# Kernel optimization log

Hardware: AMD Instinct MI355X
Metric: run time of the kernel (lower is better)

Reference implementation:

```python
import jax, jax.numpy as jnp
import numpy as np

IN_C = 256
INTER_C = 128


def _conv1x1(x_flat, w, b):
    # x_flat: [n, c_in, N]; w: [c_out, c_in]; b: [c_out] -> [n, c_out, N]
    return jnp.einsum('oc,bcn->bon', w, x_flat) + b[None, :, None]


def setup_inputs() -> dict:
    key = jax.random.key(0)
    ks = jax.random.split(key, 9)
    x = jax.random.normal(ks[0], (4, IN_C, 64, 64), dtype=jnp.float32)
    s_in = 1.0 / np.sqrt(IN_C)
    s_mid = 1.0 / np.sqrt(INTER_C)
    return {
        'x': x,
        'g_w': jax.random.uniform(ks[1], (INTER_C, IN_C), jnp.float32, -s_in, s_in),
        'g_b': jax.random.uniform(ks[2], (INTER_C,), jnp.float32, -s_in, s_in),
        'theta_w': jax.random.uniform(ks[3], (INTER_C, IN_C), jnp.float32, -s_in, s_in),
        'theta_b': jax.random.uniform(ks[4], (INTER_C,), jnp.float32, -s_in, s_in),
        'phi_w': jax.random.uniform(ks[5], (INTER_C, IN_C), jnp.float32, -s_in, s_in),
        'phi_b': jax.random.uniform(ks[6], (INTER_C,), jnp.float32, -s_in, s_in),
        'out_w': jax.random.uniform(ks[7], (IN_C, INTER_C), jnp.float32, -s_mid, s_mid),
        'out_b': jax.random.uniform(ks[8], (IN_C,), jnp.float32, -s_mid, s_mid),
    }


def reference(x, g_w, g_b, theta_w, theta_b, phi_w, phi_b, out_w, out_b):
    n, c, h, w = x.shape
    N = h * w
    x_flat = x.reshape(n, c, N)
    # 1x1-conv projections
    g_x = _conv1x1(x_flat, g_w, g_b).transpose(0, 2, 1)       # [n, N, ci]
    theta_x = _conv1x1(x_flat, theta_w, theta_b).transpose(0, 2, 1)  # [n, N, ci]
    phi_x = _conv1x1(x_flat, phi_w, phi_b)                    # [n, ci, N]
    # dot_product variant: pairwise weight normalized by N (no softmax)
    pairwise_weight = jnp.matmul(theta_x, phi_x) / N          # [n, N, N]
    y = jnp.matmul(pairwise_weight, g_x)                      # [n, N, ci]
    y = y.transpose(0, 2, 1)                                  # [n, ci, N]
    out = x_flat + _conv1x1(y, out_w, out_b)                  # residual
    return out.reshape(n, c, h, w)
```

## Files before the change

kernel.cpp:

```cpp
#include <hip/hip_runtime.h>
#include <hip/hip_bf16.h>


#define CC   256
#define NSP  4096
#define NB   4
#define KSPLIT 16

typedef __attribute__((ext_vector_type(8))) short bf16x8;
typedef __attribute__((ext_vector_type(4))) float f32x4;

#define F_BST  0
#define F_PART 512
#define F_WEND 1049088
#define H_XT   0
#define H_PG   4194304
#define H_TT   8388608
#define H_WST  10485760
#define H_OWH  10584064
#define H_W2   10616832

__device__ __forceinline__ unsigned short f2bf(float f) {
  __hip_bfloat16 h = __float2bfloat16(f);
  return __builtin_bit_cast(unsigned short, h);
}
__device__ __forceinline__ uint4 pack8(const unsigned short* h) {
  uint4 u;
  u.x = (unsigned)h[0] | ((unsigned)h[1] << 16);
  u.y = (unsigned)h[2] | ((unsigned)h[3] << 16);
  u.z = (unsigned)h[4] | ((unsigned)h[5] << 16);
  u.w = (unsigned)h[6] | ((unsigned)h[7] << 16);
  return u;
}

__device__ __forceinline__ void wave_gemm_bt(const unsigned short* __restrict__ A, int pitchA,
                                             const unsigned short* __restrict__ B, int pitchB,
                                             int K, int lane, f32x4 acc[4][4]) {
  int lm = lane & 15, lq = lane >> 4;
  const unsigned short* ap[4];
  const unsigned short* bp[4];
#pragma unroll
  for (int i = 0; i < 4; ++i) {
    ap[i] = A + (size_t)(i * 16 + lm) * pitchA + lq * 8;
    bp[i] = B + (size_t)(i * 16 + lm) * pitchB + lq * 8;
  }
  bf16x8 a0[4], b0[4];
#pragma unroll
  for (int i = 0; i < 4; ++i) {
    a0[i] = *(const bf16x8*)(ap[i]);
    b0[i] = *(const bf16x8*)(bp[i]);
  }
  for (int k = 32; k < K; k += 32) {
    bf16x8 a1[4], b1[4];
#pragma unroll
    for (int i = 0; i < 4; ++i) {
      a1[i] = *(const bf16x8*)(ap[i] + k);
      b1[i] = *(const bf16x8*)(bp[i] + k);
    }
#pragma unroll
    for (int mi = 0; mi < 4; ++mi)
#pragma unroll
      for (int ni = 0; ni < 4; ++ni)
        acc[mi][ni] = __builtin_amdgcn_mfma_f32_16x16x32_bf16(a0[mi], b0[ni], acc[mi][ni], 0, 0, 0);
#pragma unroll
    for (int i = 0; i < 4; ++i) { a0[i] = a1[i]; b0[i] = b1[i]; }
  }
#pragma unroll
  for (int mi = 0; mi < 4; ++mi)
#pragma unroll
    for (int ni = 0; ni < 4; ++ni)
      acc[mi][ni] = __builtin_amdgcn_mfma_f32_16x16x32_bf16(a0[mi], b0[ni], acc[mi][ni], 0, 0, 0);
}

__global__ __launch_bounds__(256) void kA(
    const float* __restrict__ g_w, const float* __restrict__ theta_w,
    const float* __restrict__ phi_w, const float* __restrict__ out_w,
    const float* __restrict__ g_b, const float* __restrict__ theta_b,
    const float* __restrict__ phi_b, const float* __restrict__ x,
    float* __restrict__ wsf, unsigned short* __restrict__ wsh) {
  __shared__ float T[64][65];
  int bid = blockIdx.x, t = threadIdx.x;
  if (bid < 1024) {
    int nt = bid & 63, ct = (bid >> 6) & 3, b = bid >> 8;
    int c0 = ct * 64, n0 = nt * 64;
    int r = t >> 2, j = t & 3;
    const float* xr = x + ((size_t)b * CC + c0 + r) * NSP + n0 + j * 16;
    float4 f0 = *(const float4*)(xr);
    float4 f1 = *(const float4*)(xr + 4);
    float4 f2 = *(const float4*)(xr + 8);
    float4 f3 = *(const float4*)(xr + 12);
    *(float4*)&T[r][j * 16 + 0]  = f0;
    *(float4*)&T[r][j * 16 + 4]  = f1;
    *(float4*)&T[r][j * 16 + 8]  = f2;
    *(float4*)&T[r][j * 16 + 12] = f3;
    __syncthreads();
    int nr = t >> 2, j2 = t & 3;
    unsigned short o[16];
#pragma unroll
    for (int i = 0; i < 16; ++i) o[i] = f2bf(T[j2 * 16 + i][nr]);
    size_t to = ((size_t)b * NSP + n0 + nr) * CC + c0 + j2 * 16;
    *(uint4*)(wsh + H_XT + to)     = pack8(o);
    *(uint4*)(wsh + H_XT + to + 8) = pack8(o + 8);
  } else if (bid < 1028) {
    int r0 = (bid - 1024) * 96;
    for (int i = 0; i < 96; ++i) {
      int rr = r0 + i;
      const float* src = (rr < 128) ? (g_w + (size_t)rr * CC)
                       : (rr < 256) ? (theta_w + (size_t)(rr - 128) * CC)
                                    : (phi_w + (size_t)(rr - 256) * CC);
      wsh[H_WST + (size_t)rr * CC + t] = f2bf(src[t]);
    }
  } else {
    for (int i = t; i < 32768; i += 256) wsh[H_OWH + i] = f2bf(out_w[i]);
    if (t < 128) {
      wsf[F_BST + t]       = g_b[t];
      wsf[F_BST + 128 + t] = theta_b[t];
      wsf[F_BST + 256 + t] = phi_b[t];
    }
  }
}

__global__ __launch_bounds__(256) void kB(const float* __restrict__ wsf,
                                          unsigned short* __restrict__ wsh) {
  __shared__ float bL[128];
  int bid = blockIdx.x;
  int b = bid / 96, rem = bid % 96;
  int r = rem >> 5, c = rem & 31;
  int t = threadIdx.x, w = t >> 6, lane = t & 63;
  int wm = w >> 1, wn = w & 1;
  int lm = lane & 15, lq = lane >> 4;
  if (t < 128) bL[t] = wsf[F_BST + r * 128 + t];
  __syncthreads();

  const unsigned short* A = wsh + H_WST + (size_t)(r * 128 + wm * 64) * CC;
  const unsigned short* B = wsh + H_XT + ((size_t)b * NSP + c * 128 + wn * 64) * CC;
  f32x4 acc[4][4] = {};
  wave_gemm_bt(A, CC, B, CC, 256, lane, acc);

  int colb = c * 128 + wn * 64;
  if (r == 1) {
    size_t tb = (size_t)b * 524288;
#pragma unroll
    for (int mi = 0; mi < 4; ++mi) {
      int p0 = wm * 64 + mi * 16 + lq * 4;
#pragma unroll
      for (int ni = 0; ni < 4; ++ni) {
        int col = colb + ni * 16 + lm;
        unsigned short u0 = f2bf(acc[mi][ni][0] + bL[p0 + 0]);
        unsigned short u1 = f2bf(acc[mi][ni][1] + bL[p0 + 1]);
        unsigned short u2 = f2bf(acc[mi][ni][2] + bL[p0 + 2]);
        unsigned short u3 = f2bf(acc[mi][ni][3] + bL[p0 + 3]);
        uint2 o;
        o.x = (unsigned)u0 | ((unsigned)u1 << 16);
        o.y = (unsigned)u2 | ((unsigned)u3 << 16);
        *(uint2*)(wsh + H_TT + tb + (size_t)col * 128 + p0) = o;
      }
    }
  } else {
    int rbase = (r == 0) ? 0 : 128;
    size_t pbo = (size_t)b * 1048576;
#pragma unroll
    for (int mi = 0; mi < 4; ++mi)
#pragma unroll
      for (int rr = 0; rr < 4; ++rr) {
        int rl = wm * 64 + mi * 16 + lq * 4 + rr;
        float bv = bL[rl];
        size_t rowo = pbo + (size_t)(rbase + rl) * NSP;
#pragma unroll
        for (int ni = 0; ni < 4; ++ni)
          wsh[H_PG + rowo + colb + ni * 16 + lm] = f2bf(acc[mi][ni][rr] + bv);
      }
  }
}

__global__ __launch_bounds__(256) void kC1(const unsigned short* __restrict__ wsh,
                                           float* __restrict__ wsf) {
  int bid = blockIdx.x;
  int b = bid >> 4, ks = bid & 15;
  int t = threadIdx.x, w = t >> 6, lane = t & 63;
  int lm = lane & 15, lq = lane >> 4;
  int qm = w >> 1, qn = w & 1;
  const unsigned short* A = wsh + H_PG + (size_t)b * 1048576 +
                            (size_t)(128 + qm * 64) * NSP + ks * 256;
  const unsigned short* B = wsh + H_PG + (size_t)b * 1048576 +
                            (size_t)(qn * 64) * NSP + ks * 256;
  f32x4 acc[4][4] = {};
  wave_gemm_bt(A, NSP, B, NSP, 256, lane, acc);
  float* P = wsf + F_PART + (size_t)(b * KSPLIT + ks) * 16384;
#pragma unroll
  for (int mi = 0; mi < 4; ++mi)
#pragma unroll
    for (int rr = 0; rr < 4; ++rr) {
      int p = qm * 64 + mi * 16 + lq * 4 + rr;
#pragma unroll
      for (int ni = 0; ni < 4; ++ni)
        P[p * 128 + qn * 64 + ni * 16 + lm] = acc[mi][ni][rr];
    }
}

__global__ __launch_bounds__(256) void kC2(const float* __restrict__ wsf,
                                           unsigned short* __restrict__ wsh) {
  __shared__ unsigned short Sh[128][136];
  int b = blockIdx.x;
  int t = threadIdx.x, w = t >> 6, lane = t & 63;
  int lm = lane & 15, lq = lane >> 4;

  const float* PB = wsf + F_PART + (size_t)b * KSPLIT * 16384;
#pragma unroll
  for (int e = 0; e < 16; ++e) {
    int base = (e * 256 + t) * 4;
    float4 s = {0.f, 0.f, 0.f, 0.f};
#pragma unroll
    for (int ks = 0; ks < KSPLIT; ++ks) {
      float4 p = *(const float4*)(PB + (size_t)ks * 16384 + base);
      s.x += p.x; s.y += p.y; s.z += p.z; s.w += p.w;
    }
    int pr = base >> 7, g = base & 127;
    uint2 o;
    o.x = (unsigned)f2bf(s.x) | ((unsigned)f2bf(s.y) << 16);
    o.y = (unsigned)f2bf(s.z) | ((unsigned)f2bf(s.w) << 16);
    *(uint2*)(&Sh[pr][g]) = o;
  }
  __syncthreads();

  const unsigned short* A2 = wsh + H_OWH + (size_t)(w * 64) * 128;
  f32x4 acc2[4][8] = {};
  for (int k = 0; k < 128; k += 32) {
    bf16x8 a[4], bb[8];
#pragma unroll
    for (int i = 0; i < 4; ++i)
      a[i] = *(const bf16x8*)(A2 + (size_t)(i * 16 + lm) * 128 + lq * 8 + k);
#pragma unroll
    for (int j = 0; j < 8; ++j)
      bb[j] = *(const bf16x8*)(&Sh[j * 16 + lm][lq * 8 + k]);
#pragma unroll
    for (int mi = 0; mi < 4; ++mi)
#pragma unroll
      for (int nj = 0; nj < 8; ++nj)
        acc2[mi][nj] = __builtin_amdgcn_mfma_f32_16x16x32_bf16(a[mi], bb[nj], acc2[mi][nj], 0, 0, 0);
  }
  const float inv = 1.0f / 4096.0f;
#pragma unroll
  for (int mi = 0; mi < 4; ++mi)
#pragma unroll
    for (int rr = 0; rr < 4; ++rr) {
      int i = w * 64 + mi * 16 + lq * 4 + rr;
      size_t rowo = (size_t)b * 32768 + (size_t)i * 128;
#pragma unroll
      for (int nj = 0; nj < 8; ++nj)
        wsh[H_W2 + rowo + nj * 16 + lm] = f2bf(acc2[mi][nj][rr] * inv);
    }
}

__global__ __launch_bounds__(256) void kD(const unsigned short* __restrict__ wsh,
                                          const float* __restrict__ x,
                                          const float* __restrict__ out_b,
                                          float* __restrict__ out) {
  int bid = blockIdx.x;
  int b = bid >> 6, r6 = bid & 63;
  int tm = r6 >> 5, tn = r6 & 31;
  int t = threadIdx.x, w = t >> 6, lane = t & 63;
  int wm = w >> 1, wn = w & 1;
  int rb = tm * 128 + wm * 64, cb = tn * 128 + wn * 64;
  const unsigned short* A = wsh + H_W2 + (size_t)b * 32768 + (size_t)rb * 128;
  const unsigned short* B = wsh + H_TT + (size_t)b * 524288 + (size_t)cb * 128;
  f32x4 acc[4][4] = {};
  wave_gemm_bt(A, 128, B, 128, 128, lane, acc);
  int lm = lane & 15, lq = lane >> 4;
#pragma unroll
  for (int mi = 0; mi < 4; ++mi)
#pragma unroll
    for (int rr = 0; rr < 4; ++rr) {
      int row = rb + mi * 16 + lq * 4 + rr;
      float bi = out_b[row];
#pragma unroll
      for (int ni = 0; ni < 4; ++ni) {
        int col = cb + ni * 16 + lm;
        size_t off = ((size_t)b * CC + row) * NSP + col;
        out[off] = acc[mi][ni][rr] + x[off] + bi;
      }
    }
}

extern "C" void kernel_launch(void* const* d_in, const int* in_sizes, int n_in,
                              void* d_out, int out_size, void* d_ws, size_t ws_size,
                              hipStream_t stream) {
  const float* x       = (const float*)d_in[0];
  const float* g_w     = (const float*)d_in[1];
  const float* g_b     = (const float*)d_in[2];
  const float* theta_w = (const float*)d_in[3];
  const float* theta_b = (const float*)d_in[4];
  const float* phi_w   = (const float*)d_in[5];
  const float* phi_b   = (const float*)d_in[6];
  const float* out_w   = (const float*)d_in[7];
  const float* out_b   = (const float*)d_in[8];
  float* wsf = (float*)d_ws;
  unsigned short* wsh = (unsigned short*)(wsf + F_WEND);
  float* out = (float*)d_out;

  kA<<<dim3(1029), dim3(256), 0, stream>>>(g_w, theta_w, phi_w, out_w,
                                           g_b, theta_b, phi_b, x, wsf, wsh);
  kB<<<dim3(384), dim3(256), 0, stream>>>(wsf, wsh);
  kC1<<<dim3(64), dim3(256), 0, stream>>>(wsh, wsf);
  kC2<<<dim3(4), dim3(256), 0, stream>>>(wsf, wsh);
  kD<<<dim3(256), dim3(256), 0, stream>>>(wsh, x, out_b, out);
}
```

Before: 155.7 us.

## Fuse x transpose into projection kernel and fold out_w product into output kernel

The transpose/convert of x is merged into the projection kernel, which keeps a swizzled bf16 x tile in LDS and converts fp32 weights on the fly instead of staging them in the workspace. The single-block kC2 (reduce plus out_w GEMM) is split into a parallel 64-block reduction kernel. The out_w times S product is recomputed per output block inside kD into swizzled LDS. This drops one launch and the serial 4-block stage, but kP now runs only 128 blocks doing all three projections serially, and kD repeats the small GEMM in every block.

```diff
diff --git a/kernel.cpp b/kernel.cpp
--- a/kernel.cpp
+++ b/kernel.cpp
@@ -10,15 +10,10 @@
 typedef __attribute__((ext_vector_type(8))) short bf16x8;
 typedef __attribute__((ext_vector_type(4))) float f32x4;
 
-#define F_BST  0
-#define F_PART 512
-#define F_WEND 1049088
-#define H_XT   0
-#define H_PG   4194304
-#define H_TT   8388608
-#define H_WST  10485760
-#define H_OWH  10584064
-#define H_W2   10616832
+#define F_WEND 1048576
+#define H_PG   0
+#define H_TT   4194304
+#define H_S2   6291456
 
 __device__ __forceinline__ unsigned short f2bf(float f) {
   __hip_bfloat16 h = __float2bfloat16(f);
@@ -32,6 +27,16 @@
   u.w = (unsigned)h[6] | ((unsigned)h[7] << 16);
   return u;
 }
+__device__ __forceinline__ bf16x8 ld_cvt8(const float* __restrict__ p) {
+  float4 lo = *(const float4*)p;
+  float4 hi = *(const float4*)(p + 4);
+  bf16x8 r;
+  r[0] = (short)f2bf(lo.x); r[1] = (short)f2bf(lo.y);
+  r[2] = (short)f2bf(lo.z); r[3] = (short)f2bf(lo.w);
+  r[4] = (short)f2bf(hi.x); r[5] = (short)f2bf(hi.y);
+  r[6] = (short)f2bf(hi.z); r[7] = (short)f2bf(hi.w);
+  return r;
+}
 
 __device__ __forceinline__ void wave_gemm_bt(const unsigned short* __restrict__ A, int pitchA,
                                              const unsigned short* __restrict__ B, int pitchB,
@@ -72,19 +77,26 @@
       acc[mi][ni] = __builtin_amdgcn_mfma_f32_16x16x32_bf16(a0[mi], b0[ni], acc[mi][ni], 0, 0, 0);
 }
 
-__global__ __launch_bounds__(256) void kA(
+__global__ __launch_bounds__(256) void kP(
     const float* __restrict__ g_w, const float* __restrict__ theta_w,
-    const float* __restrict__ phi_w, const float* __restrict__ out_w,
-    const float* __restrict__ g_b, const float* __restrict__ theta_b,
-    const float* __restrict__ phi_b, const float* __restrict__ x,
-    float* __restrict__ wsf, unsigned short* __restrict__ wsh) {
+    const float* __restrict__ phi_w, const float* __restrict__ g_b,
+    const float* __restrict__ theta_b, const float* __restrict__ phi_b,
+    const float* __restrict__ x, unsigned short* __restrict__ wsh) {
   __shared__ float T[64][65];
-  int bid = blockIdx.x, t = threadIdx.x;
-  if (bid < 1024) {
-    int nt = bid & 63, ct = (bid >> 6) & 3, b = bid >> 8;
-    int c0 = ct * 64, n0 = nt * 64;
+  __shared__ unsigned short XL[128 * 256];
+  __shared__ float biasL[384];
+  int bid = blockIdx.x;
+  int b = bid >> 5, c = bid & 31;
+  int t = threadIdx.x;
+  if (t < 128) {
+    biasL[t]       = g_b[t];
+    biasL[128 + t] = theta_b[t];
+    biasL[256 + t] = phi_b[t];
+  }
+  for (int s = 0; s < 8; ++s) {
+    int kb = s >> 1, nb = s & 1;
     int r = t >> 2, j = t & 3;
-    const float* xr = x + ((size_t)b * CC + c0 + r) * NSP + n0 + j * 16;
+    const float* xr = x + ((size_t)b * CC + kb * 64 + r) * NSP + c * 128 + nb * 64 + j * 16;
     float4 f0 = *(const float4*)(xr);
     float4 f1 = *(const float4*)(xr + 4);
     float4 f2 = *(const float4*)(xr + 8);
@@ -98,83 +110,94 @@
     unsigned short o[16];
 #pragma unroll
     for (int i = 0; i < 16; ++i) o[i] = f2bf(T[j2 * 16 + i][nr]);
-    size_t to = ((size_t)b * NSP + n0 + nr) * CC + c0 + j2 * 16;
-    *(uint4*)(wsh + H_XT + to)     = pack8(o);
-    *(uint4*)(wsh + H_XT + to + 8) = pack8(o + 8);
-  } else if (bid < 1028) {
-    int r0 = (bid - 1024) * 96;
-    for (int i = 0; i < 96; ++i) {
-      int rr = r0 + i;
-      const float* src = (rr < 128) ? (g_w + (size_t)rr * CC)
-                       : (rr < 256) ? (theta_w + (size_t)(rr - 128) * CC)
-                                    : (phi_w + (size_t)(rr - 256) * CC);
-      wsh[H_WST + (size_t)rr * CC + t] = f2bf(src[t]);
-    }
-  } else {
-    for (int i = t; i < 32768; i += 256) wsh[H_OWH + i] = f2bf(out_w[i]);
-    if (t < 128) {
-      wsf[F_BST + t]       = g_b[t];
-      wsf[F_BST + 128 + t] = theta_b[t];
-      wsf[F_BST + 256 + t] = phi_b[t];
-    }
-  }
-}
-
-__global__ __launch_bounds__(256) void kB(const float* __restrict__ wsf,
-                                          unsigned short* __restrict__ wsh) {
-  __shared__ float bL[128];
-  int bid = blockIdx.x;
-  int b = bid / 96, rem = bid % 96;
-  int r = rem >> 5, c = rem & 31;
-  int t = threadIdx.x, w = t >> 6, lane = t & 63;
+    int row = nb * 64 + nr;
+    int kidx = kb * 64 + j2 * 16;
+    int sw = (row & 7) << 3;
+    *(uint4*)(XL + ((row * 256 + kidx) ^ sw))     = pack8(o);
+    *(uint4*)(XL + ((row * 256 + kidx + 8) ^ sw)) = pack8(o + 8);
+    __syncthreads();
+  }
+
+  int w = t >> 6, lane = t & 63;
   int wm = w >> 1, wn = w & 1;
   int lm = lane & 15, lq = lane >> 4;
-  if (t < 128) bL[t] = wsf[F_BST + r * 128 + t];
-  __syncthreads();
-
-  const unsigned short* A = wsh + H_WST + (size_t)(r * 128 + wm * 64) * CC;
-  const unsigned short* B = wsh + H_XT + ((size_t)b * NSP + c * 128 + wn * 64) * CC;
-  f32x4 acc[4][4] = {};
-  wave_gemm_bt(A, CC, B, CC, 256, lane, acc);
-
-  int colb = c * 128 + wn * 64;
-  if (r == 1) {
-    size_t tb = (size_t)b * 524288;
-#pragma unroll
-    for (int mi = 0; mi < 4; ++mi) {
-      int p0 = wm * 64 + mi * 16 + lq * 4;
-#pragma unroll
-      for (int ni = 0; ni < 4; ++ni) {
-        int col = colb + ni * 16 + lm;
-        unsigned short u0 = f2bf(acc[mi][ni][0] + bL[p0 + 0]);
-        unsigned short u1 = f2bf(acc[mi][ni][1] + bL[p0 + 1]);
-        unsigned short u2 = f2bf(acc[mi][ni][2] + bL[p0 + 2]);
-        unsigned short u3 = f2bf(acc[mi][ni][3] + bL[p0 + 3]);
-        uint2 o;
-        o.x = (unsigned)u0 | ((unsigned)u1 << 16);
-        o.y = (unsigned)u2 | ((unsigned)u3 << 16);
-        *(uint2*)(wsh + H_TT + tb + (size_t)col * 128 + p0) = o;
-      }
-    }
-  } else {
-    int rbase = (r == 0) ? 0 : 128;
-    size_t pbo = (size_t)b * 1048576;
+  int bsw = (lm & 7) << 3;
+#pragma unroll
+  for (int r = 0; r < 3; ++r) {
+    const float* wptr = (r == 0) ? g_w : (r == 1) ? theta_w : phi_w;
+    const float* ap[4];
+    int bidx[4];
+#pragma unroll
+    for (int i = 0; i < 4; ++i) {
+      ap[i] = wptr + (size_t)(wm * 64 + i * 16 + lm) * CC + lq * 8;
+      bidx[i] = (wn * 64 + i * 16 + lm) * 256 + lq * 8;
+    }
+    f32x4 acc[4][4] = {};
+    bf16x8 a0[4], b0[4];
+#pragma unroll
+    for (int i = 0; i < 4; ++i) {
+      a0[i] = ld_cvt8(ap[i]);
+      b0[i] = *(const bf16x8*)(XL + (bidx[i] ^ bsw));
+    }
+    for (int k = 32; k < 256; k += 32) {
+      bf16x8 a1[4], b1[4];
+#pragma unroll
+      for (int i = 0; i < 4; ++i) {
+        a1[i] = ld_cvt8(ap[i] + k);
+        b1[i] = *(const bf16x8*)(XL + ((bidx[i] + k) ^ bsw));
+      }
+#pragma unroll
+      for (int mi = 0; mi < 4; ++mi)
+#pragma unroll
+        for (int ni = 0; ni < 4; ++ni)
+          acc[mi][ni] = __builtin_amdgcn_mfma_f32_16x16x32_bf16(a0[mi], b0[ni], acc[mi][ni], 0, 0, 0);
+#pragma unroll
+      for (int i = 0; i < 4; ++i) { a0[i] = a1[i]; b0[i] = b1[i]; }
+    }
 #pragma unroll
     for (int mi = 0; mi < 4; ++mi)
 #pragma unroll
-      for (int rr = 0; rr < 4; ++rr) {
-        int rl = wm * 64 + mi * 16 + lq * 4 + rr;
-        float bv = bL[rl];
-        size_t rowo = pbo + (size_t)(rbase + rl) * NSP;
-#pragma unroll
-        for (int ni = 0; ni < 4; ++ni)
-          wsh[H_PG + rowo + colb + ni * 16 + lm] = f2bf(acc[mi][ni][rr] + bv);
-      }
-  }
-}
-
-__global__ __launch_bounds__(256) void kC1(const unsigned short* __restrict__ wsh,
-                                           float* __restrict__ wsf) {
+      for (int ni = 0; ni < 4; ++ni)
+        acc[mi][ni] = __builtin_amdgcn_mfma_f32_16x16x32_bf16(a0[mi], b0[ni], acc[mi][ni], 0, 0, 0);
+
+    if (r == 1) {
+      size_t tb = (size_t)b * 524288;
+#pragma unroll
+      for (int mi = 0; mi < 4; ++mi) {
+        int p0 = wm * 64 + mi * 16 + lq * 4;
+#pragma unroll
+        for (int ni = 0; ni < 4; ++ni) {
+          int n = c * 128 + wn * 64 + ni * 16 + lm;
+          unsigned short u0 = f2bf(acc[mi][ni][0] + biasL[128 + p0 + 0]);
+          unsigned short u1 = f2bf(acc[mi][ni][1] + biasL[128 + p0 + 1]);
+          unsigned short u2 = f2bf(acc[mi][ni][2] + biasL[128 + p0 + 2]);
+          unsigned short u3 = f2bf(acc[mi][ni][3] + biasL[128 + p0 + 3]);
+          uint2 o;
+          o.x = (unsigned)u0 | ((unsigned)u1 << 16);
+          o.y = (unsigned)u2 | ((unsigned)u3 << 16);
+          *(uint2*)(wsh + H_TT + tb + (size_t)n * 128 + p0) = o;
+        }
+      }
+    } else {
+      int rbase = (r == 0) ? 0 : 128;
+      size_t pbo = (size_t)b * 1048576;
+#pragma unroll
+      for (int mi = 0; mi < 4; ++mi)
+#pragma unroll
+        for (int rr = 0; rr < 4; ++rr) {
+          int rl = wm * 64 + mi * 16 + lq * 4 + rr;
+          float bv = biasL[r * 128 + rl];
+          size_t rowo = pbo + (size_t)(rbase + rl) * NSP;
+#pragma unroll
+          for (int ni = 0; ni < 4; ++ni)
+            wsh[H_PG + rowo + c * 128 + wn * 64 + ni * 16 + lm] = f2bf(acc[mi][ni][rr] + bv);
+        }
+    }
+  }
+}
+
+__global__ __launch_bounds__(256) void kS(const unsigned short* __restrict__ wsh,
+                                          float* __restrict__ wsf) {
   int bid = blockIdx.x;
   int b = bid >> 4, ks = bid & 15;
   int t = threadIdx.x, w = t >> 6, lane = t & 63;
@@ -186,7 +209,7 @@
                             (size_t)(qn * 64) * NSP + ks * 256;
   f32x4 acc[4][4] = {};
   wave_gemm_bt(A, NSP, B, NSP, 256, lane, acc);
-  float* P = wsf + F_PART + (size_t)(b * KSPLIT + ks) * 16384;
+  float* P = wsf + (size_t)(b * KSPLIT + ks) * 16384;
 #pragma unroll
   for (int mi = 0; mi < 4; ++mi)
 #pragma unroll
@@ -198,80 +221,118 @@
     }
 }
 
-__global__ __launch_bounds__(256) void kC2(const float* __restrict__ wsf,
-                                           unsigned short* __restrict__ wsh) {
-  __shared__ unsigned short Sh[128][136];
-  int b = blockIdx.x;
-  int t = threadIdx.x, w = t >> 6, lane = t & 63;
-  int lm = lane & 15, lq = lane >> 4;
-
-  const float* PB = wsf + F_PART + (size_t)b * KSPLIT * 16384;
-#pragma unroll
-  for (int e = 0; e < 16; ++e) {
-    int base = (e * 256 + t) * 4;
-    float4 s = {0.f, 0.f, 0.f, 0.f};
-#pragma unroll
-    for (int ks = 0; ks < KSPLIT; ++ks) {
-      float4 p = *(const float4*)(PB + (size_t)ks * 16384 + base);
-      s.x += p.x; s.y += p.y; s.z += p.z; s.w += p.w;
-    }
-    int pr = base >> 7, g = base & 127;
-    uint2 o;
-    o.x = (unsigned)f2bf(s.x) | ((unsigned)f2bf(s.y) << 16);
-    o.y = (unsigned)f2bf(s.z) | ((unsigned)f2bf(s.w) << 16);
-    *(uint2*)(&Sh[pr][g]) = o;
-  }
-  __syncthreads();
-
-  const unsigned short* A2 = wsh + H_OWH + (size_t)(w * 64) * 128;
-  f32x4 acc2[4][8] = {};
-  for (int k = 0; k < 128; k += 32) {
-    bf16x8 a[4], bb[8];
-#pragma unroll
-    for (int i = 0; i < 4; ++i)
-      a[i] = *(const bf16x8*)(A2 + (size_t)(i * 16 + lm) * 128 + lq * 8 + k);
-#pragma unroll
-    for (int j = 0; j < 8; ++j)
-      bb[j] = *(const bf16x8*)(&Sh[j * 16 + lm][lq * 8 + k]);
-#pragma unroll
-    for (int mi = 0; mi < 4; ++mi)
-#pragma unroll
-      for (int nj = 0; nj < 8; ++nj)
-        acc2[mi][nj] = __builtin_amdgcn_mfma_f32_16x16x32_bf16(a[mi], bb[nj], acc2[mi][nj], 0, 0, 0);
-  }
-  const float inv = 1.0f / 4096.0f;
-#pragma unroll
-  for (int mi = 0; mi < 4; ++mi)
-#pragma unroll
-    for (int rr = 0; rr < 4; ++rr) {
-      int i = w * 64 + mi * 16 + lq * 4 + rr;
-      size_t rowo = (size_t)b * 32768 + (size_t)i * 128;
-#pragma unroll
-      for (int nj = 0; nj < 8; ++nj)
-        wsh[H_W2 + rowo + nj * 16 + lm] = f2bf(acc2[mi][nj][rr] * inv);
-    }
+__global__ __launch_bounds__(256) void kR(const float* __restrict__ wsf,
+                                          unsigned short* __restrict__ wsh) {
+  int bid = blockIdx.x;
+  int b = bid >> 4, e = bid & 15;
+  int t = threadIdx.x;
+  int base = e * 1024 + t * 4;
+  const float* PB = wsf + (size_t)b * KSPLIT * 16384;
+  float4 s = {0.f, 0.f, 0.f, 0.f};
+#pragma unroll
+  for (int ks = 0; ks < KSPLIT; ++ks) {
+    float4 p = *(const float4*)(PB + (size_t)ks * 16384 + base);
+    s.x += p.x; s.y += p.y; s.z += p.z; s.w += p.w;
+  }
+  uint2 o;
+  o.x = (unsigned)f2bf(s.x) | ((unsigned)f2bf(s.y) << 16);
+  o.y = (unsigned)f2bf(s.z) | ((unsigned)f2bf(s.w) << 16);
+  *(uint2*)(wsh + H_S2 + (size_t)b * 16384 + base) = o;
 }
 
 __global__ __launch_bounds__(256) void kD(const unsigned short* __restrict__ wsh,
+                                          const float* __restrict__ out_w,
                                           const float* __restrict__ x,
                                           const float* __restrict__ out_b,
                                           float* __restrict__ out) {
+  __shared__ unsigned short W2L[128 * 128];
   int bid = blockIdx.x;
   int b = bid >> 6, r6 = bid & 63;
   int tm = r6 >> 5, tn = r6 & 31;
   int t = threadIdx.x, w = t >> 6, lane = t & 63;
+  int lm = lane & 15, lq = lane >> 4;
+  int rb = tm * 128;
+
+  {
+    int pm = w >> 1, im = w & 1;
+    const unsigned short* As = wsh + H_S2 + (size_t)b * 16384;
+    f32x4 macc[4][4] = {};
+    for (int kk = 0; kk < 128; kk += 32) {
+      bf16x8 a[4], bb[4];
+#pragma unroll
+      for (int i = 0; i < 4; ++i) {
+        a[i]  = *(const bf16x8*)(As + (size_t)(pm * 64 + i * 16 + lm) * 128 + lq * 8 + kk);
+        bb[i] = ld_cvt8(out_w + (size_t)(rb + im * 64 + i * 16 + lm) * 128 + lq * 8 + kk);
+      }
+#pragma unroll
+      for (int mi = 0; mi < 4; ++mi)
+#pragma unroll
+        for (int ni = 0; ni < 4; ++ni)
+          macc[mi][ni] = __builtin_amdgcn_mfma_f32_16x16x32_bf16(a[mi], bb[ni], macc[mi][ni], 0, 0, 0);
+    }
+    const float inv = 1.0f / 4096.0f;
+#pragma unroll
+    for (int mi = 0; mi < 4; ++mi) {
+      int p0 = pm * 64 + mi * 16 + lq * 4;
+#pragma unroll
+      for (int ni = 0; ni < 4; ++ni) {
+        int il = im * 64 + ni * 16 + lm;
+        unsigned short u0 = f2bf(macc[mi][ni][0] * inv);
+        unsigned short u1 = f2bf(macc[mi][ni][1] * inv);
+        unsigned short u2 = f2bf(macc[mi][ni][2] * inv);
+        unsigned short u3 = f2bf(macc[mi][ni][3] * inv);
+        uint2 o;
+        o.x = (unsigned)u0 | ((unsigned)u1 << 16);
+        o.y = (unsigned)u2 | ((unsigned)u3 << 16);
+        *(uint2*)(W2L + ((il * 128 + p0) ^ ((il & 7) << 3))) = o;
+      }
+    }
+  }
+  __syncthreads();
+
   int wm = w >> 1, wn = w & 1;
-  int rb = tm * 128 + wm * 64, cb = tn * 128 + wn * 64;
-  const unsigned short* A = wsh + H_W2 + (size_t)b * 32768 + (size_t)rb * 128;
-  const unsigned short* B = wsh + H_TT + (size_t)b * 524288 + (size_t)cb * 128;
+  int cb = tn * 128 + wn * 64;
+  int asw = (lm & 7) << 3;
+  int aidx[4];
+  const unsigned short* bp[4];
+#pragma unroll
+  for (int i = 0; i < 4; ++i) {
+    aidx[i] = (wm * 64 + i * 16 + lm) * 128 + lq * 8;
+    bp[i] = wsh + H_TT + (size_t)b * 524288 + (size_t)(cb + i * 16 + lm) * 128 + lq * 8;
+  }
   f32x4 acc[4][4] = {};
-  wave_gemm_bt(A, 128, B, 128, 128, lane, acc);
-  int lm = lane & 15, lq = lane >> 4;
+  bf16x8 a0[4], b0[4];
+#pragma unroll
+  for (int i = 0; i < 4; ++i) {
+    a0[i] = *(const bf16x8*)(W2L + (aidx[i] ^ asw));
+    b0[i] = *(const bf16x8*)(bp[i]);
+  }
+  for (int k = 32; k < 128; k += 32) {
+    bf16x8 a1[4], b1[4];
+#pragma unroll
+    for (int i = 0; i < 4; ++i) {
+      a1[i] = *(const bf16x8*)(W2L + ((aidx[i] + k) ^ asw));
+      b1[i] = *(const bf16x8*)(bp[i] + k);
+    }
+#pragma unroll
+    for (int mi = 0; mi < 4; ++mi)
+#pragma unroll
+      for (int ni = 0; ni < 4; ++ni)
+        acc[mi][ni] = __builtin_amdgcn_mfma_f32_16x16x32_bf16(a0[mi], b0[ni], acc[mi][ni], 0, 0, 0);
+#pragma unroll
+    for (int i = 0; i < 4; ++i) { a0[i] = a1[i]; b0[i] = b1[i]; }
+  }
 #pragma unroll
   for (int mi = 0; mi < 4; ++mi)
 #pragma unroll
+    for (int ni = 0; ni < 4; ++ni)
+      acc[mi][ni] = __builtin_amdgcn_mfma_f32_16x16x32_bf16(a0[mi], b0[ni], acc[mi][ni], 0, 0, 0);
+
+#pragma unroll
+  for (int mi = 0; mi < 4; ++mi)
+#pragma unroll
     for (int rr = 0; rr < 4; ++rr) {
-      int row = rb + mi * 16 + lq * 4 + rr;
+      int row = rb + wm * 64 + mi * 16 + lq * 4 + rr;
       float bi = out_b[row];
 #pragma unroll
       for (int ni = 0; ni < 4; ++ni) {
@@ -298,10 +359,9 @@
   unsigned short* wsh = (unsigned short*)(wsf + F_WEND);
   float* out = (float*)d_out;
 
-  kA<<<dim3(1029), dim3(256), 0, stream>>>(g_w, theta_w, phi_w, out_w,
-                                           g_b, theta_b, phi_b, x, wsf, wsh);
-  kB<<<dim3(384), dim3(256), 0, stream>>>(wsf, wsh);
-  kC1<<<dim3(64), dim3(256), 0, stream>>>(wsh, wsf);
-  kC2<<<dim3(4), dim3(256), 0, stream>>>(wsf, wsh);
-  kD<<<dim3(256), dim3(256), 0, stream>>>(wsh, x, out_b, out);
-}
+  kP<<<dim3(128), dim3(256), 0, stream>>>(g_w, theta_w, phi_w,
+                                          g_b, theta_b, phi_b, x, wsh);
+  kS<<<dim3(64), dim3(256), 0, stream>>>(wsh, wsf);
+  kR<<<dim3(64), dim3(256), 0, stream>>>(wsf, wsh);
+  kD<<<dim3(256), dim3(256), 0, stream>>>(wsh, out_w, x, out_b, out);
+}
```

Result: faster. 138.6 us (-11.0%).
